# Kernel optimization log

Measured on AMD Instinct MI355X. Metric: run time of the kernel, lower is better.

## Reference

```python
import jax, jax.numpy as jnp
import numpy as np
import math

D_MODEL = 256
N_HEADS = 4
D_K = D_MODEL // N_HEADS
N_LAYERS = 4
PAD_ID = 0
LN_EPS = 1e-5


def _posenc(seq_len, d_model):
    pos = jnp.arange(seq_len, dtype=jnp.float32)[:, None]
    div = jnp.exp(jnp.arange(0, d_model, 2, dtype=jnp.float32) * (-math.log(10000.0) / d_model))
    pe = jnp.zeros((seq_len, d_model), dtype=jnp.float32)
    pe = pe.at[:, 0::2].set(jnp.sin(pos * div))
    pe = pe.at[:, 1::2].set(jnp.cos(pos * div))
    return pe  # (S, D)


def _layernorm(x, g, b):
    mu = jnp.mean(x, axis=-1, keepdims=True)
    var = jnp.mean((x - mu) ** 2, axis=-1, keepdims=True)
    return (x - mu) / jnp.sqrt(var + LN_EPS) * g + b


def _attention(x, mask_b11s, Wq, bq, Wk, bk, Wv, bv, Wo, bo):
    B, S, D = x.shape
    q = (x @ Wq + bq).reshape(B, S, N_HEADS, D_K)
    k = (x @ Wk + bk).reshape(B, S, N_HEADS, D_K)
    v = (x @ Wv + bv).reshape(B, S, N_HEADS, D_K)
    scores = jnp.einsum('bqhd,bkhd->bhqk', q, k) / math.sqrt(D_K)
    scores = jnp.where(mask_b11s, scores, -jnp.inf)
    attn = jax.nn.softmax(scores, axis=-1)
    out = jnp.einsum('bhqk,bkhd->bqhd', attn, v).reshape(B, S, D)
    return out @ Wo + bo


def setup_inputs() -> dict:
    key = jax.random.key(0)
    ks = jax.random.split(key, 16)
    B, S, V, D, F, L, C = 16, 2048, 32, D_MODEL, 1024, N_LAYERS, 10
    input_ids = jax.random.randint(ks[0], (B, S), 0, V, dtype=jnp.int64)
    emb = jax.random.normal(ks[1], (V, D), jnp.float32) * (D ** -0.5)
    emb = emb.at[PAD_ID].set(0.0)  # padding_idx
    sc = 0.05
    inp = {
        'input_ids': input_ids,
        'emb': emb,
        'Wq': jax.random.normal(ks[2], (L, D, D), jnp.float32) * sc,
        'bq': jnp.zeros((L, D), jnp.float32),
        'Wk': jax.random.normal(ks[3], (L, D, D), jnp.float32) * sc,
        'bk': jnp.zeros((L, D), jnp.float32),
        'Wv': jax.random.normal(ks[4], (L, D, D), jnp.float32) * sc,
        'bv': jnp.zeros((L, D), jnp.float32),
        'Wo': jax.random.normal(ks[5], (L, D, D), jnp.float32) * sc,
        'bo': jnp.zeros((L, D), jnp.float32),
        'g1': jnp.ones((L, D), jnp.float32),
        'be1': jnp.zeros((L, D), jnp.float32),
        'W1': jax.random.normal(ks[6], (L, D, F), jnp.float32) * sc,
        'b1': jnp.zeros((L, F), jnp.float32),
        'W2': jax.random.normal(ks[7], (L, F, D), jnp.float32) * sc,
        'b2': jnp.zeros((L, D), jnp.float32),
        'g2': jnp.ones((L, D), jnp.float32),
        'be2': jnp.zeros((L, D), jnp.float32),
        'Wc': jax.random.normal(ks[8], (D, C), jnp.float32) * sc,
        'bc': jnp.zeros((C,), jnp.float32),
    }
    return inp


def reference(input_ids, emb, Wq, bq, Wk, bk, Wv, bv, Wo, bo,
              g1, be1, W1, b1, W2, b2, g2, be2, Wc, bc):
    B, S = input_ids.shape
    attn_mask = (input_ids != PAD_ID)                      # (B, S) bool
    mask_b11s = attn_mask[:, None, None, :]                # (B,1,1,S)
    x = emb[input_ids] * math.sqrt(D_MODEL)                # (B,S,D)
    x = x + _posenc(S, D_MODEL)[None]
    for l in range(N_LAYERS):
        a = _attention(x, mask_b11s, Wq[l], bq[l], Wk[l], bk[l], Wv[l], bv[l], Wo[l], bo[l])
        x = _layernorm(x + a, g1[l], be1[l])
        ff = jax.nn.relu(x @ W1[l] + b1[l]) @ W2[l] + b2[l]
        x = _layernorm(x + ff, g2[l], be2[l])
    # mean pooling over non-pad tokens
    m = attn_mask.astype(jnp.float32)[:, :, None]          # (B,S,1)
    pooled = jnp.sum(x * m, axis=1) / jnp.clip(jnp.sum(m, axis=1), 1e-9)
    logits = pooled @ Wc + bc                              # (B, num_classes)
    return logits
```

## Files before the change

kernel.cpp:

```cpp
#include <hip/hip_runtime.h>
#include <hip/hip_bf16.h>
#include <math.h>

#define D_MODEL 256
#define NHEADS 4
#define DK 64
#define NLAYERS 4
#define FFDIM 1024
#define BB 16
#define SS 2048
#define NTOK (BB*SS)

#define QSCALE 0.18033688011112042f
#define MASKNEG -30000.0f

typedef __attribute__((ext_vector_type(8))) short bf16x8;
typedef __attribute__((ext_vector_type(4))) short s16x4;
typedef __attribute__((ext_vector_type(4))) float f32x4;

__device__ __forceinline__ short f2bf(float f) {
    __hip_bfloat16 h = __float2bfloat16(f);
    return *reinterpret_cast<short*>(&h);
}
__device__ __forceinline__ float bf2f(short s) {
    unsigned u = ((unsigned)(unsigned short)s) << 16;
    return __uint_as_float(u);
}

__global__ void embed_kernel(const int* __restrict__ ids, const float* __restrict__ emb,
                             float* __restrict__ x, short* __restrict__ xb) {
    int idx = blockIdx.x * 256 + threadIdx.x;
    int tok = idx >> 8;
    int d   = idx & 255;
    int s   = tok & (SS - 1);
    int id  = ids[tok];
    float e = emb[id * D_MODEL + d] * 16.0f;
    float i2 = (float)((d >> 1) << 1);
    float div = expf(i2 * (-9.210340371976184f / 256.0f));
    float ang = (float)s * div;
    float pe = (d & 1) ? cosf(ang) : sinf(ang);
    float val = e + pe;
    x[idx] = val;
    xb[idx] = f2bf(val);
}

__global__ void wprep_kernel(const float* __restrict__ Wq, const float* __restrict__ Wk,
                             const float* __restrict__ Wv, const float* __restrict__ Wo,
                             const float* __restrict__ W1, const float* __restrict__ W2,
                             short* __restrict__ wqkv, short* __restrict__ wto,
                             short* __restrict__ w1t, short* __restrict__ w2t) {
    int wid = blockIdx.y, l = blockIdx.z, tile = blockIdx.x;
    int K = (wid == 5) ? 1024 : 256;
    int M = (wid == 4) ? 1024 : 256;
    int tiles = (K >> 6) * (M >> 6);
    if (tile >= tiles) return;
    const float* src; short* dst;
    float scale = (wid == 0) ? QSCALE : 1.0f;
    switch (wid) {
        case 0: src = Wq; dst = wqkv + (size_t)l*196608;            break;
        case 1: src = Wk; dst = wqkv + (size_t)l*196608 + 65536;    break;
        case 2: src = Wv; dst = wqkv + (size_t)l*196608 + 131072;   break;
        case 3: src = Wo; dst = wto + (size_t)l*65536;              break;
        case 4: src = W1; dst = w1t + (size_t)l*262144;             break;
        default: src = W2; dst = w2t + (size_t)l*262144;            break;
    }
    src += (size_t)l * K * M;
    int tm = tile % (M >> 6), tk = tile / (M >> 6);

    __shared__ short t_s[64][68];
    int tid = threadIdx.x;
    #pragma unroll
    for (int u = 0; u < 16; ++u) {
        int e = tid + u * 256;
        int r = e >> 6, c = e & 63;
        t_s[c][r] = f2bf(src[(size_t)(tk*64 + r) * M + tm*64 + c] * scale);
    }
    __syncthreads();
    #pragma unroll
    for (int u = 0; u < 4; ++u) {
        int e = tid + u * 256;
        int r = e >> 4, c4 = (e & 15) * 4;
        s16x4 v;
        v[0] = t_s[r][c4]; v[1] = t_s[r][c4+1]; v[2] = t_s[r][c4+2]; v[3] = t_s[r][c4+3];
        *(s16x4*)&dst[(size_t)(tm*64 + r) * K + tk*64 + c4] = v;
    }
}

__global__ void bprep_kernel(const float* __restrict__ bq, const float* __restrict__ bk,
                             const float* __restrict__ bv, float* __restrict__ bqkv) {
    int idx = blockIdx.x * 256 + threadIdx.x;
    if (idx >= NLAYERS * 768) return;
    int l = idx / 768, j = idx % 768;
    float v;
    if (j < 256) v = bq[l*256 + j] * QSCALE;
    else if (j < 512) v = bk[l*256 + j - 256];
    else v = bv[l*256 + j - 512];
    bqkv[idx] = v;
}

template<int RELU, int VSPLIT>
__global__ __launch_bounds__(256) void gemm_bf16_kernel(
        const short* __restrict__ A, const short* __restrict__ Wt,
        const float* __restrict__ bias, short* __restrict__ Cout,
        short* __restrict__ vt, int N, int K, int M) {
    __shared__ short A_s[128][72];
    __shared__ short B_s[128][72];
    int tid = threadIdx.x;
    int w = tid >> 6, lane = tid & 63;
    int lr = lane & 15, lg = lane >> 4;
    int wr = w >> 1, wc = w & 1;
    int rowBase = blockIdx.x * 128;
    int colBase = blockIdx.y * 128;

    f32x4 acc[4][4];
    #pragma unroll
    for (int m = 0; m < 4; ++m)
        #pragma unroll
        for (int n = 0; n < 4; ++n)
            acc[m][n] = (f32x4){0.f, 0.f, 0.f, 0.f};

    for (int kt = 0; kt < K; kt += 64) {
        #pragma unroll
        for (int u = 0; u < 4; ++u) {
            int e = tid + u * 256;
            int r = e >> 3, c8 = (e & 7) * 8;
            *(bf16x8*)&A_s[r][c8] = *(const bf16x8*)(A + (size_t)(rowBase + r) * K + kt + c8);
        }
        #pragma unroll
        for (int u = 0; u < 4; ++u) {
            int e = tid + u * 256;
            int r = e >> 3, c8 = (e & 7) * 8;
            *(bf16x8*)&B_s[r][c8] = *(const bf16x8*)(Wt + (size_t)(colBase + r) * K + kt + c8);
        }
        __syncthreads();
        #pragma unroll
        for (int ks = 0; ks < 2; ++ks) {
            bf16x8 af[4], bfr[4];
            #pragma unroll
            for (int m = 0; m < 4; ++m)
                af[m] = *(const bf16x8*)&A_s[wr*64 + m*16 + lr][ks*32 + lg*8];
            #pragma unroll
            for (int n = 0; n < 4; ++n)
                bfr[n] = *(const bf16x8*)&B_s[wc*64 + n*16 + lr][ks*32 + lg*8];
            #pragma unroll
            for (int m = 0; m < 4; ++m)
                #pragma unroll
                for (int n = 0; n < 4; ++n)
                    acc[m][n] = __builtin_amdgcn_mfma_f32_16x16x32_bf16(af[m], bfr[n], acc[m][n], 0, 0, 0);
        }
        __syncthreads();
    }

    #pragma unroll
    for (int m = 0; m < 4; ++m) {
        int row = rowBase + wr*64 + m*16 + lg*4;
        #pragma unroll
        for (int n = 0; n < 4; ++n) {
            int col = colBase + wc*64 + n*16 + lr;
            float bv = bias[col];
            if (VSPLIT && col >= 512) {
                int hh = (col - 512) >> 6, dl = (col - 512) & 63;
                int bb = row >> 11, s0 = row & 2047;
                s16x4 ow;
                #pragma unroll
                for (int r = 0; r < 4; ++r) ow[r] = f2bf(acc[m][n][r] + bv);
                *(s16x4*)&vt[((size_t)(bb * NHEADS + hh) * DK + dl) * SS + s0] = ow;
            } else {
                #pragma unroll
                for (int r = 0; r < 4; ++r) {
                    float vv = acc[m][n][r] + bv;
                    if (RELU) vv = fmaxf(vv, 0.0f);
                    Cout[(size_t)(row + r) * M + col] = f2bf(vv);
                }
            }
        }
    }
}

__global__ __launch_bounds__(256) void gemm_ln_kernel(
        const short* __restrict__ A, const short* __restrict__ Wt,
        const float* __restrict__ bias, const float* __restrict__ resid,
        const float* __restrict__ g, const float* __restrict__ be,
        float* __restrict__ xf, short* __restrict__ xb, int K) {
    __shared__ short A_s[64][72];
    __shared__ short B_s[256][72];
    __shared__ float red_s[2][4][64];
    __shared__ float mu_s[64], rs_s[64];
    int tid = threadIdx.x;
    int w = tid >> 6, lane = tid & 63;
    int lr = lane & 15, lg = lane >> 4;
    int rowBase = blockIdx.x * 64;
    int colW = w * 64;

    f32x4 acc[4][4];
    #pragma unroll
    for (int m = 0; m < 4; ++m)
        #pragma unroll
        for (int n = 0; n < 4; ++n)
            acc[m][n] = (f32x4){0.f, 0.f, 0.f, 0.f};

    for (int kt = 0; kt < K; kt += 64) {
        #pragma unroll
        for (int u = 0; u < 2; ++u) {
            int e = tid + u * 256;
            int r = e >> 3, c8 = (e & 7) * 8;
            *(bf16x8*)&A_s[r][c8] = *(const bf16x8*)(A + (size_t)(rowBase + r) * K + kt + c8);
        }
        #pragma unroll
        for (int u = 0; u < 8; ++u) {
            int e = tid + u * 256;
            int r = e >> 3, c8 = (e & 7) * 8;
            *(bf16x8*)&B_s[r][c8] = *(const bf16x8*)(Wt + (size_t)r * K + kt + c8);
        }
        __syncthreads();
        #pragma unroll
        for (int ks = 0; ks < 2; ++ks) {
            bf16x8 af[4], bfr[4];
            #pragma unroll
            for (int m = 0; m < 4; ++m)
                af[m] = *(const bf16x8*)&A_s[m*16 + lr][ks*32 + lg*8];
            #pragma unroll
            for (int n = 0; n < 4; ++n)
                bfr[n] = *(const bf16x8*)&B_s[colW + n*16 + lr][ks*32 + lg*8];
            #pragma unroll
            for (int m = 0; m < 4; ++m)
                #pragma unroll
                for (int n = 0; n < 4; ++n)
                    acc[m][n] = __builtin_amdgcn_mfma_f32_16x16x32_bf16(af[m], bfr[n], acc[m][n], 0, 0, 0);
        }
        __syncthreads();
    }

    #pragma unroll
    for (int m = 0; m < 4; ++m) {
        #pragma unroll
        for (int n = 0; n < 4; ++n) {
            int col = colW + n*16 + lr;
            float bv = bias[col];
            #pragma unroll
            for (int r = 0; r < 4; ++r) {
                int row = rowBase + m*16 + lg*4 + r;
                acc[m][n][r] += bv + resid[(size_t)row * 256 + col];
            }
        }
    }
    #pragma unroll
    for (int m = 0; m < 4; ++m) {
        #pragma unroll
        for (int r = 0; r < 4; ++r) {
            float sum = acc[m][0][r] + acc[m][1][r] + acc[m][2][r] + acc[m][3][r];
            float sq  = acc[m][0][r]*acc[m][0][r] + acc[m][1][r]*acc[m][1][r]
                      + acc[m][2][r]*acc[m][2][r] + acc[m][3][r]*acc[m][3][r];
            #pragma unroll
            for (int off = 1; off < 16; off <<= 1) {
                sum += __shfl_xor(sum, off);
                sq  += __shfl_xor(sq, off);
            }
            if (lr == 0) {
                red_s[0][w][m*16 + lg*4 + r] = sum;
                red_s[1][w][m*16 + lg*4 + r] = sq;
            }
        }
    }
    __syncthreads();
    if (tid < 64) {
        float s = red_s[0][0][tid] + red_s[0][1][tid] + red_s[0][2][tid] + red_s[0][3][tid];
        float q = red_s[1][0][tid] + red_s[1][1][tid] + red_s[1][2][tid] + red_s[1][3][tid];
        float mu = s * (1.0f/256.0f);
        float var = q * (1.0f/256.0f) - mu*mu;
        mu_s[tid] = mu;
        rs_s[tid] = rsqrtf(var + 1e-5f);
    }
    __syncthreads();
    #pragma unroll
    for (int m = 0; m < 4; ++m) {
        #pragma unroll
        for (int n = 0; n < 4; ++n) {
            int col = colW + n*16 + lr;
            float gv = g[col], bev = be[col];
            #pragma unroll
            for (int r = 0; r < 4; ++r) {
                int rloc = m*16 + lg*4 + r;
                int row = rowBase + rloc;
                float o = (acc[m][n][r] - mu_s[rloc]) * rs_s[rloc] * gv + bev;
                xf[(size_t)row * 256 + col] = o;
                xb[(size_t)row * 256 + col] = f2bf(o);
            }
        }
    }
}

__global__ __launch_bounds__(256) void flash_mfma_kernel(
        const short* __restrict__ qkv, const short* __restrict__ vt_g,
        const int* __restrict__ ids, short* __restrict__ o_part,
        float* __restrict__ l_part) {
    __shared__ short k_s[64][68];
    __shared__ short vt_s[64][68];
    __shared__ short p_s[4][16][68];
    __shared__ float madd_s[64];

    int bid = blockIdx.x;
    int work = (bid & 7) * 256 + (bid >> 3);
    int u = work & 1023;
    int sp = work >> 10;
    int qb = u & 15, h = (u >> 4) & 3, b = u >> 6;

    int tid = threadIdx.x;
    int w = tid >> 6, lane = tid & 63;
    int lr = lane & 15, lg = lane >> 4;
    int g = lr >> 2;

    const short* qp = qkv + (size_t)b * SS * 768 + h * DK;
    const short* kp = qp + 256;
    const short* vtp = vt_g + (size_t)(b * NHEADS + h) * DK * SS;

    bf16x8 qf[2][2];
    #pragma unroll
    for (int s = 0; s < 2; ++s) {
        int qrow = qb*128 + w*32 + s*16 + lr;
        #pragma unroll
        for (int ks = 0; ks < 2; ++ks)
            qf[s][ks] = *(const bf16x8*)(qp + (size_t)qrow * 768 + lg*8 + ks*32);
    }

    f32x4 o[2][4];
    float l_i[2] = {0.0f, 0.0f};
    #pragma unroll
    for (int s = 0; s < 2; ++s)
        #pragma unroll
        for (int dt = 0; dt < 4; ++dt)
            o[s][dt] = (f32x4){0.f, 0.f, 0.f, 0.f};

    int r0 = tid >> 3, c8 = (tid & 7) * 8;
    const int kb0 = sp * 16;

    bf16x8 kr[2], vr[2];
    int idv = 1;
    #pragma unroll
    for (int uu = 0; uu < 2; ++uu) {
        kr[uu] = *(const bf16x8*)(kp + (size_t)(kb0*64 + r0 + uu*32) * 768 + c8);
        vr[uu] = *(const bf16x8*)(vtp + (size_t)(r0 + uu*32) * SS + kb0*64 + c8);
    }
    if (tid < 64) idv = ids[b*SS + kb0*64 + tid];

    for (int kb = kb0; kb < kb0 + 16; ++kb) {
        __syncthreads();
        #pragma unroll
        for (int uu = 0; uu < 2; ++uu) {
            *(bf16x8*)&k_s[r0 + uu*32][c8] = kr[uu];
            *(bf16x8*)&vt_s[r0 + uu*32][c8] = vr[uu];
        }
        if (tid < 64)
            madd_s[tid] = (idv != 0) ? 0.0f : MASKNEG;
        if (kb + 1 < kb0 + 16) {
            #pragma unroll
            for (int uu = 0; uu < 2; ++uu) {
                kr[uu] = *(const bf16x8*)(kp + (size_t)((kb+1)*64 + r0 + uu*32) * 768 + c8);
                vr[uu] = *(const bf16x8*)(vtp + (size_t)(r0 + uu*32) * SS + (kb+1)*64 + c8);
            }
            if (tid < 64) idv = ids[b*SS + (kb+1)*64 + tid];
        }
        __syncthreads();

        f32x4 madd4[4];
        #pragma unroll
        for (int t = 0; t < 4; ++t)
            madd4[t] = *(const f32x4*)&madd_s[16*t + 4*lg];

        f32x4 sc[2][4];
        __builtin_amdgcn_s_setprio(1);
        #pragma unroll
        for (int t = 0; t < 4; ++t) {
            bf16x8 kf0 = *(const bf16x8*)&k_s[t*16 + lr][lg*8];
            bf16x8 kf1 = *(const bf16x8*)&k_s[t*16 + lr][lg*8 + 32];
            #pragma unroll
            for (int s = 0; s < 2; ++s) {
                f32x4 a = __builtin_amdgcn_mfma_f32_16x16x32_bf16(kf0, qf[s][0], madd4[t], 0, 0, 0);
                a = __builtin_amdgcn_mfma_f32_16x16x32_bf16(kf1, qf[s][1], a, 0, 0, 0);
                sc[s][t] = a;
            }
        }
        __builtin_amdgcn_s_setprio(0);

        bf16x8 pa[2][2];
        #pragma unroll
        for (int s = 0; s < 2; ++s) {
            float pv[4][4];
            #pragma unroll
            for (int t = 0; t < 4; ++t)
                #pragma unroll
                for (int r = 0; r < 4; ++r)
                    pv[t][r] = __builtin_amdgcn_exp2f(sc[s][t][r]);
            float st0 = (pv[0][0] + pv[0][1]) + (pv[0][2] + pv[0][3]);
            float st1 = (pv[1][0] + pv[1][1]) + (pv[1][2] + pv[1][3]);
            float st2 = (pv[2][0] + pv[2][1]) + (pv[2][2] + pv[2][3]);
            float st3 = (pv[3][0] + pv[3][1]) + (pv[3][2] + pv[3][3]);
            l_i[s] += (st0 + st1) + (st2 + st3);

            #pragma unroll
            for (int t = 0; t < 4; ++t) {
                s16x4 pw;
                #pragma unroll
                for (int r = 0; r < 4; ++r) pw[r] = f2bf(pv[t][r]);
                *(s16x4*)&p_s[w][lr][16*(t ^ g) + 4*lg] = pw;
            }
            #pragma unroll
            for (int ks = 0; ks < 2; ++ks) {
                int t0 = 2*ks + (lg >> 1);
                pa[s][ks] = *(const bf16x8*)&p_s[w][lr][16*(t0 ^ g) + 8*(lg & 1)];
            }
        }

        __builtin_amdgcn_s_setprio(1);
        #pragma unroll
        for (int dt = 0; dt < 4; ++dt) {
            #pragma unroll
            for (int ks = 0; ks < 2; ++ks) {
                bf16x8 va = *(const bf16x8*)&vt_s[dt*16 + lr][ks*32 + lg*8];
                o[0][dt] = __builtin_amdgcn_mfma_f32_16x16x32_bf16(va, pa[0][ks], o[0][dt], 0, 0, 0);
                o[1][dt] = __builtin_amdgcn_mfma_f32_16x16x32_bf16(va, pa[1][ks], o[1][dt], 0, 0, 0);
            }
        }
        __builtin_amdgcn_s_setprio(0);
    }

    size_t pidx = (size_t)u * 2 + sp;
    #pragma unroll
    for (int s = 0; s < 2; ++s) {
        float l = l_i[s];
        l += __shfl_xor(l, 16);
        l += __shfl_xor(l, 32);
        int ql = w*32 + s*16 + lr;
        #pragma unroll
        for (int dt = 0; dt < 4; ++dt) {
            s16x4 ow;
            #pragma unroll
            for (int r = 0; r < 4; ++r) ow[r] = f2bf(o[s][dt][r]);
            *(s16x4*)&o_part[pidx*8192 + (size_t)ql*64 + dt*16 + 4*lg] = ow;
        }
        if (lg == 0) l_part[pidx*128 + ql] = l;
    }
}

__global__ __launch_bounds__(256) void combine_kernel(
        const short* __restrict__ o_part, const float* __restrict__ l_part,
        short* __restrict__ out) {
    int u = blockIdx.x;
    int qb = u & 15, h = (u >> 4) & 3, b = u >> 6;
    __shared__ float inv_s[128];
    int tid = threadIdx.x;
    if (tid < 128)
        inv_s[tid] = 1.0f / (l_part[(size_t)u*256 + tid] + l_part[(size_t)u*256 + 128 + tid]);
    __syncthreads();
    const short* p0 = o_part + (size_t)u * 16384;
    const short* p1 = p0 + 8192;
    #pragma unroll
    for (int i = 0; i < 4; ++i) {
        int idx = (i*256 + tid) * 8;
        int ql = idx >> 6, d0 = idx & 63;
        bf16x8 a = *(const bf16x8*)(p0 + idx);
        bf16x8 c = *(const bf16x8*)(p1 + idx);
        float inv = inv_s[ql];
        bf16x8 ow;
        #pragma unroll
        for (int j = 0; j < 8; ++j)
            ow[j] = f2bf((bf2f(a[j]) + bf2f(c[j])) * inv);
        int row = b*SS + qb*128 + ql;
        *(bf16x8*)&out[(size_t)row * 256 + h*DK + d0] = ow;
    }
}

__global__ void pool1_kernel(const float* __restrict__ x, const int* __restrict__ ids,
                             float* __restrict__ partial) {
    int b = blockIdx.x >> 4, chunk = blockIdx.x & 15;
    int d = threadIdx.x;
    float acc = 0.0f;
    int s0 = chunk * 128;
    for (int s = s0; s < s0 + 128; ++s) {
        if (ids[b*SS + s] != 0) acc += x[(size_t)(b*SS + s) * D_MODEL + d];
    }
    partial[(size_t)(b*16 + chunk) * D_MODEL + d] = acc;
}

__global__ void pool2_kernel(const float* __restrict__ partial, const int* __restrict__ ids,
                             float* __restrict__ pooled) {
    int b = blockIdx.x;
    int d = threadIdx.x;
    float acc = 0.0f;
    for (int c = 0; c < 16; ++c) acc += partial[(size_t)(b*16 + c) * D_MODEL + d];
    int cnt = 0;
    for (int s = threadIdx.x; s < SS; s += 256) cnt += (ids[b*SS + s] != 0);
    __shared__ int cs[256];
    cs[threadIdx.x] = cnt;
    __syncthreads();
    for (int off = 128; off > 0; off >>= 1) {
        if (threadIdx.x < off) cs[threadIdx.x] += cs[threadIdx.x + off];
        __syncthreads();
    }
    float total = (float)cs[0];
    pooled[b * D_MODEL + d] = acc / fmaxf(total, 1e-9f);
}

__global__ void cls_kernel(const float* __restrict__ pooled, const float* __restrict__ Wc,
                           const float* __restrict__ bc, float* __restrict__ outp) {
    int t = threadIdx.x;
    if (t >= BB * 10) return;
    int b = t / 10, c = t % 10;
    float acc = bc[c];
    for (int d = 0; d < D_MODEL; ++d)
        acc += pooled[b * D_MODEL + d] * Wc[d * 10 + c];
    outp[t] = acc;
}

extern "C" void kernel_launch(void* const* d_in, const int* in_sizes, int n_in,
                              void* d_out, int out_size, void* d_ws, size_t ws_size,
                              hipStream_t stream) {
    const int*   ids = (const int*)  d_in[0];
    const float* emb = (const float*)d_in[1];
    const float* Wq  = (const float*)d_in[2];
    const float* bq  = (const float*)d_in[3];
    const float* Wk  = (const float*)d_in[4];
    const float* bk  = (const float*)d_in[5];
    const float* Wv  = (const float*)d_in[6];
    const float* bv  = (const float*)d_in[7];
    const float* Wo  = (const float*)d_in[8];
    const float* bo  = (const float*)d_in[9];
    const float* g1  = (const float*)d_in[10];
    const float* be1 = (const float*)d_in[11];
    const float* W1  = (const float*)d_in[12];
    const float* b1  = (const float*)d_in[13];
    const float* W2  = (const float*)d_in[14];
    const float* b2  = (const float*)d_in[15];
    const float* g2  = (const float*)d_in[16];
    const float* be2 = (const float*)d_in[17];
    const float* Wc  = (const float*)d_in[18];
    const float* bc  = (const float*)d_in[19];
    float* outp = (float*)d_out;

    const size_t TD = (size_t)NTOK * D_MODEL;
    float* ws   = (float*)d_ws;
    float* x    = ws;
    short* sb   = (short*)(ws + TD);
    short* xb   = sb;
    short* qkv  = sb + TD;
    short* t0   = sb + 4*TD;
    short* vt_g = sb + 5*TD;
    short* o_part = sb + 6*TD;
    short* hh   = qkv;
    short* wqkv = sb + 8*TD;
    short* wto  = wqkv + (size_t)NLAYERS*196608;
    short* w1t  = wto  + (size_t)NLAYERS*65536;
    short* w2t  = w1t  + (size_t)NLAYERS*262144;
    float* bqkv = (float*)(w2t + (size_t)NLAYERS*262144);
    float* l_part = bqkv + NLAYERS*768;
    float* poolp = l_part + 262144;
    float* pooled = poolp + 65536;

    wprep_kernel<<<dim3(64, 6, NLAYERS), 256, 0, stream>>>(Wq, Wk, Wv, Wo, W1, W2,
                                                           wqkv, wto, w1t, w2t);
    bprep_kernel<<<12, 256, 0, stream>>>(bq, bk, bv, bqkv);
    embed_kernel<<<NTOK, 256, 0, stream>>>(ids, emb, x, xb);

    dim3 gQKV(NTOK/128, 768/128);
    dim3 gF1 (NTOK/128, FFDIM/128);

    for (int l = 0; l < NLAYERS; ++l) {
        gemm_bf16_kernel<0,1><<<gQKV, 256, 0, stream>>>(xb, wqkv + (size_t)l*196608, bqkv + l*768,
                                                        qkv, vt_g, NTOK, D_MODEL, 768);
        flash_mfma_kernel<<<2048, 256, 0, stream>>>(qkv, vt_g, ids, o_part, l_part);
        combine_kernel<<<1024, 256, 0, stream>>>(o_part, l_part, t0);
        gemm_ln_kernel<<<NTOK/64, 256, 0, stream>>>(t0, wto + (size_t)l*65536, bo + l*D_MODEL,
                                                    x, g1 + l*D_MODEL, be1 + l*D_MODEL,
                                                    x, xb, D_MODEL);
        gemm_bf16_kernel<1,0><<<gF1, 256, 0, stream>>>(xb, w1t + (size_t)l*262144, b1 + l*FFDIM,
                                                       hh, nullptr, NTOK, D_MODEL, FFDIM);
        gemm_ln_kernel<<<NTOK/64, 256, 0, stream>>>(hh, w2t + (size_t)l*262144, b2 + l*D_MODEL,
                                                    x, g2 + l*D_MODEL, be2 + l*D_MODEL,
                                                    x, xb, FFDIM);
    }

    pool1_kernel<<<BB*16, 256, 0, stream>>>(x, ids, poolp);
    pool2_kernel<<<BB, 256, 0, stream>>>(poolp, ids, pooled);
    cls_kernel<<<1, 256, 0, stream>>>(pooled, Wc, bc, outp);
}
```

Baseline: 1.027 ms.

## Fuse split-KV combine into out-projection GEMM and register-prefetch GEMM tiles

Removes the separate combine kernel by having the Wo GEMM+LayerNorm kernel read the two flash-attention partial outputs and row sums directly, normalising them while staging A into shared memory. This avoids writing and re-reading the intermediate t0 buffer and one launch per layer. Both GEMM kernels also prefetch the next K-tile into registers while computing the current one, with the barrier moved to the loop start. The cost is higher register pressure and extra conversion arithmetic inside the GEMM staging path.

```diff
diff --git a/kernel.cpp b/kernel.cpp
--- a/kernel.cpp
+++ b/kernel.cpp
@@ -119,18 +119,32 @@
         for (int n = 0; n < 4; ++n)
             acc[m][n] = (f32x4){0.f, 0.f, 0.f, 0.f};
 
+    bf16x8 ar[4], br[4];
+    #pragma unroll
+    for (int u = 0; u < 4; ++u) {
+        int e = tid + u * 256;
+        int r = e >> 3, c8 = (e & 7) * 8;
+        ar[u] = *(const bf16x8*)(A + (size_t)(rowBase + r) * K + c8);
+        br[u] = *(const bf16x8*)(Wt + (size_t)(colBase + r) * K + c8);
+    }
+
     for (int kt = 0; kt < K; kt += 64) {
+        __syncthreads();
         #pragma unroll
         for (int u = 0; u < 4; ++u) {
             int e = tid + u * 256;
             int r = e >> 3, c8 = (e & 7) * 8;
-            *(bf16x8*)&A_s[r][c8] = *(const bf16x8*)(A + (size_t)(rowBase + r) * K + kt + c8);
-        }
-        #pragma unroll
-        for (int u = 0; u < 4; ++u) {
-            int e = tid + u * 256;
-            int r = e >> 3, c8 = (e & 7) * 8;
-            *(bf16x8*)&B_s[r][c8] = *(const bf16x8*)(Wt + (size_t)(colBase + r) * K + kt + c8);
+            *(bf16x8*)&A_s[r][c8] = ar[u];
+            *(bf16x8*)&B_s[r][c8] = br[u];
+        }
+        if (kt + 64 < K) {
+            #pragma unroll
+            for (int u = 0; u < 4; ++u) {
+                int e = tid + u * 256;
+                int r = e >> 3, c8 = (e & 7) * 8;
+                ar[u] = *(const bf16x8*)(A + (size_t)(rowBase + r) * K + kt + 64 + c8);
+                br[u] = *(const bf16x8*)(Wt + (size_t)(colBase + r) * K + kt + 64 + c8);
+            }
         }
         __syncthreads();
         #pragma unroll
@@ -148,7 +162,6 @@
                 for (int n = 0; n < 4; ++n)
                     acc[m][n] = __builtin_amdgcn_mfma_f32_16x16x32_bf16(af[m], bfr[n], acc[m][n], 0, 0, 0);
         }
-        __syncthreads();
     }
 
     #pragma unroll
@@ -177,8 +190,10 @@
     }
 }
 
+template<int ACOMB>
 __global__ __launch_bounds__(256) void gemm_ln_kernel(
-        const short* __restrict__ A, const short* __restrict__ Wt,
+        const short* __restrict__ A, const short* __restrict__ o_part,
+        const float* __restrict__ l_part, const short* __restrict__ Wt,
         const float* __restrict__ bias, const float* __restrict__ resid,
         const float* __restrict__ g, const float* __restrict__ be,
         float* __restrict__ xf, short* __restrict__ xb, int K) {
@@ -199,18 +214,84 @@
         for (int n = 0; n < 4; ++n)
             acc[m][n] = (f32x4){0.f, 0.f, 0.f, 0.f};
 
+    int rA = (tid >> 3);
+    int cA = (tid & 7) * 8;
+    int rowA0 = rowBase + rA;
+    int b0 = rowA0 >> 11, sr0 = rowA0 & 2047, qb0 = sr0 >> 7, ql0 = sr0 & 127;
+    int rowA1 = rowBase + rA + 32;
+    int b1 = rowA1 >> 11, sr1 = rowA1 & 2047, qb1 = sr1 >> 7, ql1 = sr1 & 127;
+
+    bf16x8 a0r[2], a1r[2], ar[2], br[8];
+    float li[2];
+
+    if (ACOMB) {
+        int uidx0 = b0*64 + qb0;
+        int uidx1 = b1*64 + qb1;
+        size_t base0 = (size_t)uidx0 * 16384 + (size_t)ql0*64 + cA;
+        size_t base1 = (size_t)uidx1 * 16384 + (size_t)ql1*64 + cA;
+        a0r[0] = *(const bf16x8*)(o_part + base0);
+        a1r[0] = *(const bf16x8*)(o_part + base0 + 8192);
+        a0r[1] = *(const bf16x8*)(o_part + base1);
+        a1r[1] = *(const bf16x8*)(o_part + base1 + 8192);
+        li[0] = l_part[uidx0*256 + ql0] + l_part[uidx0*256 + 128 + ql0];
+        li[1] = l_part[uidx1*256 + ql1] + l_part[uidx1*256 + 128 + ql1];
+    } else {
+        ar[0] = *(const bf16x8*)(A + (size_t)rowA0 * K + cA);
+        ar[1] = *(const bf16x8*)(A + (size_t)rowA1 * K + cA);
+    }
+    #pragma unroll
+    for (int u = 0; u < 8; ++u) {
+        int e = tid + u * 256;
+        int r = e >> 3, c8 = (e & 7) * 8;
+        br[u] = *(const bf16x8*)(Wt + (size_t)r * K + c8);
+    }
+
     for (int kt = 0; kt < K; kt += 64) {
-        #pragma unroll
-        for (int u = 0; u < 2; ++u) {
-            int e = tid + u * 256;
-            int r = e >> 3, c8 = (e & 7) * 8;
-            *(bf16x8*)&A_s[r][c8] = *(const bf16x8*)(A + (size_t)(rowBase + r) * K + kt + c8);
+        __syncthreads();
+        if (ACOMB) {
+            #pragma unroll
+            for (int u = 0; u < 2; ++u) {
+                float inv = 1.0f / li[u];
+                bf16x8 t;
+                #pragma unroll
+                for (int j = 0; j < 8; ++j)
+                    t[j] = f2bf((bf2f(a0r[u][j]) + bf2f(a1r[u][j])) * inv);
+                *(bf16x8*)&A_s[rA + u*32][cA] = t;
+            }
+        } else {
+            *(bf16x8*)&A_s[rA][cA] = ar[0];
+            *(bf16x8*)&A_s[rA + 32][cA] = ar[1];
         }
         #pragma unroll
         for (int u = 0; u < 8; ++u) {
             int e = tid + u * 256;
             int r = e >> 3, c8 = (e & 7) * 8;
-            *(bf16x8*)&B_s[r][c8] = *(const bf16x8*)(Wt + (size_t)r * K + kt + c8);
+            *(bf16x8*)&B_s[r][c8] = br[u];
+        }
+        if (kt + 64 < K) {
+            int kn = kt + 64;
+            if (ACOMB) {
+                int h = kn >> 6;
+                int uidx0 = b0*64 + h*16 + qb0;
+                int uidx1 = b1*64 + h*16 + qb1;
+                size_t base0 = (size_t)uidx0 * 16384 + (size_t)ql0*64 + cA;
+                size_t base1 = (size_t)uidx1 * 16384 + (size_t)ql1*64 + cA;
+                a0r[0] = *(const bf16x8*)(o_part + base0);
+                a1r[0] = *(const bf16x8*)(o_part + base0 + 8192);
+                a0r[1] = *(const bf16x8*)(o_part + base1);
+                a1r[1] = *(const bf16x8*)(o_part + base1 + 8192);
+                li[0] = l_part[uidx0*256 + ql0] + l_part[uidx0*256 + 128 + ql0];
+                li[1] = l_part[uidx1*256 + ql1] + l_part[uidx1*256 + 128 + ql1];
+            } else {
+                ar[0] = *(const bf16x8*)(A + (size_t)rowA0 * K + kn + cA);
+                ar[1] = *(const bf16x8*)(A + (size_t)rowA1 * K + kn + cA);
+            }
+            #pragma unroll
+            for (int u = 0; u < 8; ++u) {
+                int e = tid + u * 256;
+                int r = e >> 3, c8 = (e & 7) * 8;
+                br[u] = *(const bf16x8*)(Wt + (size_t)r * K + kn + c8);
+            }
         }
         __syncthreads();
         #pragma unroll
@@ -228,7 +309,6 @@
                 for (int n = 0; n < 4; ++n)
                     acc[m][n] = __builtin_amdgcn_mfma_f32_16x16x32_bf16(af[m], bfr[n], acc[m][n], 0, 0, 0);
         }
-        __syncthreads();
     }
 
     #pragma unroll
@@ -439,34 +519,6 @@
             *(s16x4*)&o_part[pidx*8192 + (size_t)ql*64 + dt*16 + 4*lg] = ow;
         }
         if (lg == 0) l_part[pidx*128 + ql] = l;
-    }
-}
-
-__global__ __launch_bounds__(256) void combine_kernel(
-        const short* __restrict__ o_part, const float* __restrict__ l_part,
-        short* __restrict__ out) {
-    int u = blockIdx.x;
-    int qb = u & 15, h = (u >> 4) & 3, b = u >> 6;
-    __shared__ float inv_s[128];
-    int tid = threadIdx.x;
-    if (tid < 128)
-        inv_s[tid] = 1.0f / (l_part[(size_t)u*256 + tid] + l_part[(size_t)u*256 + 128 + tid]);
-    __syncthreads();
-    const short* p0 = o_part + (size_t)u * 16384;
-    const short* p1 = p0 + 8192;
-    #pragma unroll
-    for (int i = 0; i < 4; ++i) {
-        int idx = (i*256 + tid) * 8;
-        int ql = idx >> 6, d0 = idx & 63;
-        bf16x8 a = *(const bf16x8*)(p0 + idx);
-        bf16x8 c = *(const bf16x8*)(p1 + idx);
-        float inv = inv_s[ql];
-        bf16x8 ow;
-        #pragma unroll
-        for (int j = 0; j < 8; ++j)
-            ow[j] = f2bf((bf2f(a[j]) + bf2f(c[j])) * inv);
-        int row = b*SS + qb*128 + ql;
-        *(bf16x8*)&out[(size_t)row * 256 + h*DK + d0] = ow;
     }
 }
 
@@ -543,7 +595,6 @@
     short* sb   = (short*)(ws + TD);
     short* xb   = sb;
     short* qkv  = sb + TD;
-    short* t0   = sb + 4*TD;
     short* vt_g = sb + 5*TD;
     short* o_part = sb + 6*TD;
     short* hh   = qkv;
@@ -568,15 +619,16 @@
         gemm_bf16_kernel<0,1><<<gQKV, 256, 0, stream>>>(xb, wqkv + (size_t)l*196608, bqkv + l*768,
                                                         qkv, vt_g, NTOK, D_MODEL, 768);
         flash_mfma_kernel<<<2048, 256, 0, stream>>>(qkv, vt_g, ids, o_part, l_part);
-        combine_kernel<<<1024, 256, 0, stream>>>(o_part, l_part, t0);
-        gemm_ln_kernel<<<NTOK/64, 256, 0, stream>>>(t0, wto + (size_t)l*65536, bo + l*D_MODEL,
-                                                    x, g1 + l*D_MODEL, be1 + l*D_MODEL,
-                                                    x, xb, D_MODEL);
+        gemm_ln_kernel<1><<<NTOK/64, 256, 0, stream>>>(nullptr, o_part, l_part,
+                                                       wto + (size_t)l*65536, bo + l*D_MODEL,
+                                                       x, g1 + l*D_MODEL, be1 + l*D_MODEL,
+                                                       x, xb, D_MODEL);
         gemm_bf16_kernel<1,0><<<gF1, 256, 0, stream>>>(xb, w1t + (size_t)l*262144, b1 + l*FFDIM,
                                                        hh, nullptr, NTOK, D_MODEL, FFDIM);
-        gemm_ln_kernel<<<NTOK/64, 256, 0, stream>>>(hh, w2t + (size_t)l*262144, b2 + l*D_MODEL,
-                                                    x, g2 + l*D_MODEL, be2 + l*D_MODEL,
-                                                    x, xb, FFDIM);
+        gemm_ln_kernel<0><<<NTOK/64, 256, 0, stream>>>(hh, nullptr, nullptr,
+                                                       w2t + (size_t)l*262144, b2 + l*D_MODEL,
+                                                       x, g2 + l*D_MODEL, be2 + l*D_MODEL,
+                                                       x, xb, FFDIM);
     }
 
     pool1_kernel<<<BB*16, 256, 0, stream>>>(x, ids, poolp);
```

After: 1.043 ms. Within noise of the previous version (+1.5%).

## Load K/V fragments directly from global memory in flash attention, drop LDS staging

Applied to the files above, without the earlier changes.

The flash attention kernel no longer stages K and V^T tiles through shared memory with register prefetch and two barriers per key block. Each wave now reads its MFMA operands for K, V^T and a precomputed additive mask straight from global memory, relying on L1/L2 to serve the four waves that share them. A new prep kernel builds the float mask once from the token ids. This removes the barriers and LDS traffic, but each wave now issues its own uncoalesced global loads with no explicit prefetch, so latency is exposed unless occupancy hides it.

```diff
diff --git a/kernel.cpp b/kernel.cpp
--- a/kernel.cpp
+++ b/kernel.cpp
@@ -42,6 +42,11 @@
     float val = e + pe;
     x[idx] = val;
     xb[idx] = f2bf(val);
+}
+
+__global__ void maddprep_kernel(const int* __restrict__ ids, float* __restrict__ maddg) {
+    int idx = blockIdx.x * 256 + threadIdx.x;
+    if (idx < NTOK) maddg[idx] = (ids[idx] != 0) ? 0.0f : MASKNEG;
 }
 
 __global__ void wprep_kernel(const float* __restrict__ Wq, const float* __restrict__ Wk,
@@ -292,12 +297,9 @@
 
 __global__ __launch_bounds__(256) void flash_mfma_kernel(
         const short* __restrict__ qkv, const short* __restrict__ vt_g,
-        const int* __restrict__ ids, short* __restrict__ o_part,
+        const float* __restrict__ maddg, short* __restrict__ o_part,
         float* __restrict__ l_part) {
-    __shared__ short k_s[64][68];
-    __shared__ short vt_s[64][68];
     __shared__ short p_s[4][16][68];
-    __shared__ float madd_s[64];
 
     int bid = blockIdx.x;
     int work = (bid & 7) * 256 + (bid >> 3);
@@ -313,6 +315,7 @@
     const short* qp = qkv + (size_t)b * SS * 768 + h * DK;
     const short* kp = qp + 256;
     const short* vtp = vt_g + (size_t)(b * NHEADS + h) * DK * SS;
+    const float* mp = maddg + b * SS;
 
     bf16x8 qf[2][2];
     #pragma unroll
@@ -331,48 +334,21 @@
         for (int dt = 0; dt < 4; ++dt)
             o[s][dt] = (f32x4){0.f, 0.f, 0.f, 0.f};
 
-    int r0 = tid >> 3, c8 = (tid & 7) * 8;
     const int kb0 = sp * 16;
 
-    bf16x8 kr[2], vr[2];
-    int idv = 1;
-    #pragma unroll
-    for (int uu = 0; uu < 2; ++uu) {
-        kr[uu] = *(const bf16x8*)(kp + (size_t)(kb0*64 + r0 + uu*32) * 768 + c8);
-        vr[uu] = *(const bf16x8*)(vtp + (size_t)(r0 + uu*32) * SS + kb0*64 + c8);
-    }
-    if (tid < 64) idv = ids[b*SS + kb0*64 + tid];
-
     for (int kb = kb0; kb < kb0 + 16; ++kb) {
-        __syncthreads();
-        #pragma unroll
-        for (int uu = 0; uu < 2; ++uu) {
-            *(bf16x8*)&k_s[r0 + uu*32][c8] = kr[uu];
-            *(bf16x8*)&vt_s[r0 + uu*32][c8] = vr[uu];
-        }
-        if (tid < 64)
-            madd_s[tid] = (idv != 0) ? 0.0f : MASKNEG;
-        if (kb + 1 < kb0 + 16) {
-            #pragma unroll
-            for (int uu = 0; uu < 2; ++uu) {
-                kr[uu] = *(const bf16x8*)(kp + (size_t)((kb+1)*64 + r0 + uu*32) * 768 + c8);
-                vr[uu] = *(const bf16x8*)(vtp + (size_t)(r0 + uu*32) * SS + (kb+1)*64 + c8);
-            }
-            if (tid < 64) idv = ids[b*SS + (kb+1)*64 + tid];
-        }
-        __syncthreads();
-
         f32x4 madd4[4];
         #pragma unroll
         for (int t = 0; t < 4; ++t)
-            madd4[t] = *(const f32x4*)&madd_s[16*t + 4*lg];
+            madd4[t] = *(const f32x4*)(mp + kb*64 + 16*t + 4*lg);
 
         f32x4 sc[2][4];
         __builtin_amdgcn_s_setprio(1);
         #pragma unroll
         for (int t = 0; t < 4; ++t) {
-            bf16x8 kf0 = *(const bf16x8*)&k_s[t*16 + lr][lg*8];
-            bf16x8 kf1 = *(const bf16x8*)&k_s[t*16 + lr][lg*8 + 32];
+            const short* krow = kp + (size_t)(kb*64 + t*16 + lr) * 768 + lg*8;
+            bf16x8 kf0 = *(const bf16x8*)krow;
+            bf16x8 kf1 = *(const bf16x8*)(krow + 32);
             #pragma unroll
             for (int s = 0; s < 2; ++s) {
                 f32x4 a = __builtin_amdgcn_mfma_f32_16x16x32_bf16(kf0, qf[s][0], madd4[t], 0, 0, 0);
@@ -414,9 +390,10 @@
         __builtin_amdgcn_s_setprio(1);
         #pragma unroll
         for (int dt = 0; dt < 4; ++dt) {
+            const short* vrow = vtp + (size_t)(dt*16 + lr) * SS + kb*64;
             #pragma unroll
             for (int ks = 0; ks < 2; ++ks) {
-                bf16x8 va = *(const bf16x8*)&vt_s[dt*16 + lr][ks*32 + lg*8];
+                bf16x8 va = *(const bf16x8*)(vrow + ks*32 + lg*8);
                 o[0][dt] = __builtin_amdgcn_mfma_f32_16x16x32_bf16(va, pa[0][ks], o[0][dt], 0, 0, 0);
                 o[1][dt] = __builtin_amdgcn_mfma_f32_16x16x32_bf16(va, pa[1][ks], o[1][dt], 0, 0, 0);
             }
@@ -553,12 +530,14 @@
     short* w2t  = w1t  + (size_t)NLAYERS*262144;
     float* bqkv = (float*)(w2t + (size_t)NLAYERS*262144);
     float* l_part = bqkv + NLAYERS*768;
-    float* poolp = l_part + 262144;
+    float* maddg  = l_part + 262144;
+    float* poolp  = maddg + NTOK;
     float* pooled = poolp + 65536;
 
     wprep_kernel<<<dim3(64, 6, NLAYERS), 256, 0, stream>>>(Wq, Wk, Wv, Wo, W1, W2,
                                                            wqkv, wto, w1t, w2t);
     bprep_kernel<<<12, 256, 0, stream>>>(bq, bk, bv, bqkv);
+    maddprep_kernel<<<NTOK/256, 256, 0, stream>>>(ids, maddg);
     embed_kernel<<<NTOK, 256, 0, stream>>>(ids, emb, x, xb);
 
     dim3 gQKV(NTOK/128, 768/128);
@@ -567,7 +546,7 @@
     for (int l = 0; l < NLAYERS; ++l) {
         gemm_bf16_kernel<0,1><<<gQKV, 256, 0, stream>>>(xb, wqkv + (size_t)l*196608, bqkv + l*768,
                                                         qkv, vt_g, NTOK, D_MODEL, 768);
-        flash_mfma_kernel<<<2048, 256, 0, stream>>>(qkv, vt_g, ids, o_part, l_part);
+        flash_mfma_kernel<<<2048, 256, 0, stream>>>(qkv, vt_g, maddg, o_part, l_part);
         combine_kernel<<<1024, 256, 0, stream>>>(o_part, l_part, t0);
         gemm_ln_kernel<<<NTOK/64, 256, 0, stream>>>(t0, wto + (size_t)l*65536, bo + l*D_MODEL,
                                                     x, g1 + l*D_MODEL, be1 + l*D_MODEL,
```

Result: slower. 1.699 ms (+65.4%).
